# Optimization experiments

Hardware: AMD Instinct MI355X
Metric: run time of the kernel (lower is better)

Reference implementation:

```python
import jax, jax.numpy as jnp
import numpy as np

PATCH = 12
IN_CH = 1
EMBED = 96
K_NEIGH = 5
N_NODES = 1024
B = 4
L_TIME = 2016  # 12 * 168 patches
CIN = IN_CH * (K_NEIGH + 1)


def setup_inputs() -> dict:
    key = jax.random.key(0)
    k1, k2, k3, k4 = jax.random.split(key, 4)
    long_term_history = jax.random.normal(k1, (B, N_NODES, IN_CH, L_TIME), dtype=jnp.float32)
    # positive adjacency weights (used as multinomial sampling probabilities)
    adj_mx = jax.random.uniform(k2, (N_NODES, N_NODES), dtype=jnp.float32, minval=1e-3, maxval=1.0)
    # Conv2d(in=CIN, out=EMBED, kernel=(PATCH,1)) -> weight [EMBED, CIN, PATCH]
    conv_w = jax.random.normal(k3, (EMBED, CIN, PATCH), dtype=jnp.float32) * 0.02
    conv_b = jax.random.normal(k4, (EMBED,), dtype=jnp.float32) * 0.02
    return {"long_term_history": long_term_history, "adj_mx": adj_mx,
            "conv_w": conv_w, "conv_b": conv_b}


def _sample_k_neighbors(adj_mx, k, key):
    # per-row multinomial with replacement via the Gumbel-max trick
    logits = jnp.log(adj_mx)                      # row-normalization is a constant shift
    g = jax.random.gumbel(key, (adj_mx.shape[0], k, adj_mx.shape[1]), dtype=adj_mx.dtype)
    return jnp.argmax(logits[:, None, :] + g, axis=-1)  # [N, k] int


def reference(long_term_history, adj_mx, conv_w, conv_b):
    b, n, c, lt = long_term_history.shape
    # adj_adjust_u = 1, adj_adjust_v = 0 (adjust_adj_mx=False) -> adjusted adj == adj
    sampled = _sample_k_neighbors(adj_mx, K_NEIGH, jax.random.key(42))  # [N, K]
    # batched neighbor gather: [B, N, K, C, L] -> [B, N, K*C, L]
    nb = long_term_history[:, sampled].reshape(b, n, K_NEIGH * c, lt)
    data = jnp.concatenate([long_term_history, nb], axis=2)  # [B, N, (K+1)*C, L]
    # patchify conv: kernel (PATCH,1), stride (PATCH,1) == per-patch GEMM
    p = lt // PATCH
    patches = data.reshape(b, n, CIN, p, PATCH)              # [B,N,Cin,P,patch]
    out = jnp.einsum('bncpt,oct->bnop', patches, conv_w) + conv_b[None, None, :, None]
    return out  # [B, N, EMBED, P]
```

## Files before the change

kernel.cpp:

```cpp
#include <hip/hip_runtime.h>
#include <cstdint>
#include <cstddef>

#define N_NODES 1024
#define K_NEIGH 5
#define L_TIME  2016
#define PATCHSZ 12
#define EMBED   96
#define CINX    6
#define P_CNT   168
#define KDOT    72
#define OUT_PER_BN (EMBED * P_CNT)

#define WS_WH 24576
#define WS_WL (24576 + 18432)

typedef __attribute__((ext_vector_type(8))) short   bf16x8;
typedef __attribute__((ext_vector_type(4))) float   f32x4;
typedef __attribute__((ext_vector_type(4))) unsigned int u32x4;

__device__ __forceinline__ uint32_t f2bf_bits(float f) {
  uint32_t u = __float_as_uint(f);
  return (u + 0x7fffu + ((u >> 16) & 1u)) >> 16;
}
__device__ __forceinline__ float bf_hi_f(uint32_t hb) { return __uint_as_float(hb << 16); }

__device__ __forceinline__ uint32_t rotl32(uint32_t x, int r) {
  return (x << r) | (x >> (32 - r));
}
__device__ __forceinline__ uint32_t threefry_bits(uint32_t hi, uint32_t lo) {
  const uint32_t ks0 = 0u, ks1 = 42u;
  const uint32_t ks2 = ks0 ^ ks1 ^ 0x1BD11BDAu;
  uint32_t x0 = hi + ks0, x1 = lo + ks1;
#define TF_ROUND(r) { x0 += x1; x1 = rotl32(x1, (r)); x1 ^= x0; }
  TF_ROUND(13) TF_ROUND(15) TF_ROUND(26) TF_ROUND(6)
  x0 += ks1; x1 += ks2 + 1u;
  TF_ROUND(17) TF_ROUND(29) TF_ROUND(16) TF_ROUND(24)
  x0 += ks2; x1 += ks0 + 2u;
  TF_ROUND(13) TF_ROUND(15) TF_ROUND(26) TF_ROUND(6)
  x0 += ks0; x1 += ks1 + 3u;
  TF_ROUND(17) TF_ROUND(29) TF_ROUND(16) TF_ROUND(24)
  x0 += ks1; x1 += ks2 + 4u;
  TF_ROUND(13) TF_ROUND(15) TF_ROUND(26) TF_ROUND(6)
  x0 += ks2; x1 += ks0 + 5u;
#undef TF_ROUND
  return x0 ^ x1;
}
__device__ __forceinline__ float gumbel_from_bits(uint32_t bits) {
  float f = __uint_as_float((bits >> 9) | 0x3f800000u) - 1.0f;
  f = fmaxf(f, 1.17549435e-38f);
  return -logf(-logf(f));
}

__global__ __launch_bounds__(256)
void wpack_kernel(const float* __restrict__ wgt, char* __restrict__ ws) {
  const int tid = threadIdx.x;
  for (int t = tid; t < 1152; t += 256) {
    const int L  = t & 63;
    const int mk = t >> 6;
    const int kc = mk % 3;
    const int m  = mk / 3;
    const int o  = m * 16 + (L & 15);
    const int kbase = kc * 32 + (L >> 4) * 8;
    uint32_t hb[8], lb[8];
    #pragma unroll
    for (int j = 0; j < 8; ++j) {
      const int k = kbase + j;
      float v = (k < KDOT) ? wgt[o * KDOT + k] : 0.0f;
      hb[j] = f2bf_bits(v);
      lb[j] = f2bf_bits(v - bf_hi_f(hb[j]));
    }
    u32x4 ph, pl;
    #pragma unroll
    for (int i = 0; i < 4; ++i) {
      ph[i] = hb[2*i] | (hb[2*i+1] << 16);
      pl[i] = lb[2*i] | (lb[2*i+1] << 16);
    }
    *reinterpret_cast<u32x4*>(ws + WS_WH + mk * 1024 + L * 16) = ph;
    *reinterpret_cast<u32x4*>(ws + WS_WL + mk * 1024 + L * 16) = pl;
  }
}

__global__ __launch_bounds__(1024)
void sample_kernel(const float* __restrict__ adj, int* __restrict__ sampled) {
  const int n = blockIdx.x;
  const int tid = threadIdx.x;
  const float la = logf(adj[(size_t)n * N_NODES + tid]);

  float best[K_NEIGH];
  int   bestj[K_NEIGH];
  #pragma unroll
  for (int k = 0; k < K_NEIGH; ++k) {
    uint32_t bits = threefry_bits(0u, (uint32_t)((n * K_NEIGH + k) * N_NODES + tid));
    best[k] = la + gumbel_from_bits(bits);
    bestj[k] = tid;
  }
  #pragma unroll
  for (int k = 0; k < K_NEIGH; ++k) {
    #pragma unroll
    for (int off = 32; off > 0; off >>= 1) {
      float ov = __shfl_down(best[k], off);
      int   oj = __shfl_down(bestj[k], off);
      if (ov > best[k] || (ov == best[k] && oj < bestj[k])) { best[k] = ov; bestj[k] = oj; }
    }
  }
  __shared__ float sv[16][K_NEIGH];
  __shared__ int   sj[16][K_NEIGH];
  if ((tid & 63) == 0) {
    #pragma unroll
    for (int k = 0; k < K_NEIGH; ++k) { sv[tid >> 6][k] = best[k]; sj[tid >> 6][k] = bestj[k]; }
  }
  __syncthreads();
  if (tid < K_NEIGH) {
    float b = sv[0][tid];
    int  bj = sj[0][tid];
    #pragma unroll
    for (int w = 1; w < 16; ++w) {
      if (sv[w][tid] > b || (sv[w][tid] == b && sj[w][tid] < bj)) { b = sv[w][tid]; bj = sj[w][tid]; }
    }
    sampled[n * K_NEIGH + tid] = bj;
  }
}

__device__ __forceinline__ const float* sel_row(const float* r0, const float* r1,
                                                const float* r2, const float* r3,
                                                const float* r4, const float* r5,
                                                int c) {
  const float* p = r0;
  p = (c == 1) ? r1 : p;
  p = (c == 2) ? r2 : p;
  p = (c == 3) ? r3 : p;
  p = (c == 4) ? r4 : p;
  p = (c == 5) ? r5 : p;
  return p;
}

__global__ __launch_bounds__(256)
void embed_kernel(const float* __restrict__ hist, const char* __restrict__ ws,
                  const float* __restrict__ bias, const int* __restrict__ sampled,
                  float* __restrict__ out) {
  const int tid  = threadIdx.x;
  const int L    = tid & 63;
  const int wave = tid >> 6;
  const int g    = L >> 4;
  const int col  = L & 15;

  bf16x8 wh[18], wl[18];
  #pragma unroll
  for (int mk = 0; mk < 18; ++mk) {
    wh[mk] = __builtin_bit_cast(bf16x8, *reinterpret_cast<const u32x4*>(ws + WS_WH + mk*1024 + L*16));
    wl[mk] = __builtin_bit_cast(bf16x8, *reinterpret_cast<const u32x4*>(ws + WS_WL + mk*1024 + L*16));
  }
  f32x4 bv[6];
  #pragma unroll
  for (int m = 0; m < 6; ++m)
    #pragma unroll
    for (int i = 0; i < 4; ++i)
      bv[m][i] = bias[m * 16 + g * 4 + i];

  for (int bn = blockIdx.x; bn < 4 * N_NODES; bn += 512) {
    const int n = bn & (N_NODES - 1);
    const int b = bn >> 10;
    const float* r0 = hist + (size_t)bn * L_TIME;
    const float* r1 = hist + ((size_t)b * N_NODES + sampled[n * K_NEIGH + 0]) * L_TIME;
    const float* r2 = hist + ((size_t)b * N_NODES + sampled[n * K_NEIGH + 1]) * L_TIME;
    const float* r3 = hist + ((size_t)b * N_NODES + sampled[n * K_NEIGH + 2]) * L_TIME;
    const float* r4 = hist + ((size_t)b * N_NODES + sampled[n * K_NEIGH + 3]) * L_TIME;
    const float* r5 = hist + ((size_t)b * N_NODES + sampled[n * K_NEIGH + 4]) * L_TIME;
    float* outbn = out + (size_t)bn * OUT_PER_BN;

    const float* a0[3];
    const float* a1[3];
    bool okk[3];
    #pragma unroll
    for (int kc = 0; kc < 3; ++kc) {
      const int gk = kc * 32 + g * 8;
      okk[kc] = (gk < KDOT);
      const int c0 = gk / 12,       t0 = gk - c0 * 12;
      const int c1 = (gk + 4) / 12, t1 = (gk + 4) - c1 * 12;
      a0[kc] = sel_row(r0, r1, r2, r3, r4, r5, c0) + t0;
      a1[kc] = sel_row(r0, r1, r2, r3, r4, r5, c1) + t1;
    }

    for (int ntl = wave; ntl < 11; ntl += 4) {
      const int p = ntl * 16 + col;
      const bool pok = (p < P_CNT);
      f32x4 acc[6];
      #pragma unroll
      for (int m = 0; m < 6; ++m) acc[m] = bv[m];

      #pragma unroll
      for (int kc = 0; kc < 3; ++kc) {
        u32x4 ph = {0,0,0,0}, pl = {0,0,0,0};
        if (okk[kc] && pok) {
          const float4 f0 = *reinterpret_cast<const float4*>(a0[kc] + p * PATCHSZ);
          const float4 f1 = *reinterpret_cast<const float4*>(a1[kc] + p * PATCHSZ);
          const float v[8] = {f0.x, f0.y, f0.z, f0.w, f1.x, f1.y, f1.z, f1.w};
          uint32_t hb[8], lb[8];
          #pragma unroll
          for (int j = 0; j < 8; ++j) {
            hb[j] = f2bf_bits(v[j]);
            lb[j] = f2bf_bits(v[j] - bf_hi_f(hb[j]));
          }
          #pragma unroll
          for (int i = 0; i < 4; ++i) {
            ph[i] = hb[2*i] | (hb[2*i+1] << 16);
            pl[i] = lb[2*i] | (lb[2*i+1] << 16);
          }
        }
        const bf16x8 xh = __builtin_bit_cast(bf16x8, ph);
        const bf16x8 xl = __builtin_bit_cast(bf16x8, pl);
        #pragma unroll
        for (int m = 0; m < 6; ++m) {
          acc[m] = __builtin_amdgcn_mfma_f32_16x16x32_bf16(wh[m*3+kc], xh, acc[m], 0, 0, 0);
          acc[m] = __builtin_amdgcn_mfma_f32_16x16x32_bf16(wh[m*3+kc], xl, acc[m], 0, 0, 0);
          acc[m] = __builtin_amdgcn_mfma_f32_16x16x32_bf16(wl[m*3+kc], xh, acc[m], 0, 0, 0);
        }
      }
      if (pok) {
        #pragma unroll
        for (int m = 0; m < 6; ++m) {
          const int o = m * 16 + g * 4;
          #pragma unroll
          for (int i = 0; i < 4; ++i)
            __builtin_nontemporal_store(acc[m][i], &outbn[(size_t)(o + i) * P_CNT + p]);
        }
      }
    }
  }
}

extern "C" void kernel_launch(void* const* d_in, const int* in_sizes, int n_in,
                              void* d_out, int out_size, void* d_ws, size_t ws_size,
                              hipStream_t stream) {
  const float* hist = (const float*)d_in[0];
  const float* adj  = (const float*)d_in[1];
  const float* wgt  = (const float*)d_in[2];
  const float* bias = (const float*)d_in[3];
  float* out = (float*)d_out;
  char* ws   = (char*)d_ws;
  int* sampled = (int*)d_ws;

  wpack_kernel<<<dim3(1), dim3(256), 0, stream>>>(wgt, ws);
  sample_kernel<<<dim3(N_NODES), dim3(1024), 0, stream>>>(adj, sampled);
  embed_kernel<<<dim3(512), dim3(256), 0, stream>>>(hist, ws, bias, sampled, out);
}
```

Baseline: 461.7 us.

## Stage packed weights in LDS and launch one block per (batch,node)

Moves the packed hi/lo bf16 weight fragments and the bias from per-thread registers into shared memory. This frees registers so launch_bounds can request 4 blocks per SM, and each of the 4096 (batch,node) pairs now gets its own block instead of a grid-stride loop over 512 blocks. Row offsets become 32-bit indices, and the bias is added at store time instead of preloading the accumulators. In exchange, every block reloads 36KB of weights from global into LDS, and the inner MFMA loop now issues LDS reads.

Result: no change. 467.9 us (+1.3%).

```diff
diff --git a/kernel.cpp b/kernel.cpp
--- a/kernel.cpp
+++ b/kernel.cpp
@@ -122,11 +122,10 @@
   }
 }
 
-__device__ __forceinline__ const float* sel_row(const float* r0, const float* r1,
-                                                const float* r2, const float* r3,
-                                                const float* r4, const float* r5,
-                                                int c) {
-  const float* p = r0;
+__device__ __forceinline__ uint32_t sel6(uint32_t r0, uint32_t r1, uint32_t r2,
+                                         uint32_t r3, uint32_t r4, uint32_t r5,
+                                         int c) {
+  uint32_t p = r0;
   p = (c == 1) ? r1 : p;
   p = (c == 2) ? r2 : p;
   p = (c == 3) ? r3 : p;
@@ -135,66 +134,65 @@
   return p;
 }
 
-__global__ __launch_bounds__(256)
+__global__ __launch_bounds__(256, 4)
 void embed_kernel(const float* __restrict__ hist, const char* __restrict__ ws,
                   const float* __restrict__ bias, const int* __restrict__ sampled,
                   float* __restrict__ out) {
+  __shared__ __align__(16) char smem[36864 + 384];
+  u32x4* Wl = reinterpret_cast<u32x4*>(smem);
+  float* Bl = reinterpret_cast<float*>(smem + 36864);
+
   const int tid  = threadIdx.x;
   const int L    = tid & 63;
   const int wave = tid >> 6;
   const int g    = L >> 4;
   const int col  = L & 15;
 
-  bf16x8 wh[18], wl[18];
-  #pragma unroll
-  for (int mk = 0; mk < 18; ++mk) {
-    wh[mk] = __builtin_bit_cast(bf16x8, *reinterpret_cast<const u32x4*>(ws + WS_WH + mk*1024 + L*16));
-    wl[mk] = __builtin_bit_cast(bf16x8, *reinterpret_cast<const u32x4*>(ws + WS_WL + mk*1024 + L*16));
-  }
-  f32x4 bv[6];
-  #pragma unroll
-  for (int m = 0; m < 6; ++m)
-    #pragma unroll
-    for (int i = 0; i < 4; ++i)
-      bv[m][i] = bias[m * 16 + g * 4 + i];
-
-  for (int bn = blockIdx.x; bn < 4 * N_NODES; bn += 512) {
-    const int n = bn & (N_NODES - 1);
-    const int b = bn >> 10;
-    const float* r0 = hist + (size_t)bn * L_TIME;
-    const float* r1 = hist + ((size_t)b * N_NODES + sampled[n * K_NEIGH + 0]) * L_TIME;
-    const float* r2 = hist + ((size_t)b * N_NODES + sampled[n * K_NEIGH + 1]) * L_TIME;
-    const float* r3 = hist + ((size_t)b * N_NODES + sampled[n * K_NEIGH + 2]) * L_TIME;
-    const float* r4 = hist + ((size_t)b * N_NODES + sampled[n * K_NEIGH + 3]) * L_TIME;
-    const float* r5 = hist + ((size_t)b * N_NODES + sampled[n * K_NEIGH + 4]) * L_TIME;
-    float* outbn = out + (size_t)bn * OUT_PER_BN;
-
-    const float* a0[3];
-    const float* a1[3];
-    bool okk[3];
-    #pragma unroll
-    for (int kc = 0; kc < 3; ++kc) {
-      const int gk = kc * 32 + g * 8;
-      okk[kc] = (gk < KDOT);
-      const int c0 = gk / 12,       t0 = gk - c0 * 12;
-      const int c1 = (gk + 4) / 12, t1 = (gk + 4) - c1 * 12;
-      a0[kc] = sel_row(r0, r1, r2, r3, r4, r5, c0) + t0;
-      a1[kc] = sel_row(r0, r1, r2, r3, r4, r5, c1) + t1;
-    }
-
-    for (int ntl = wave; ntl < 11; ntl += 4) {
+  for (int i = tid; i < 2304; i += 256)
+    Wl[i] = *reinterpret_cast<const u32x4*>(ws + WS_WH + (size_t)i * 16);
+  if (tid < EMBED) Bl[tid] = bias[tid];
+
+  const int bn = blockIdx.x;
+  const int n  = bn & (N_NODES - 1);
+  const int b  = bn >> 10;
+
+  const uint32_t r0 = (uint32_t)bn * L_TIME;
+  const uint32_t r1 = ((uint32_t)b * N_NODES + (uint32_t)sampled[n * K_NEIGH + 0]) * L_TIME;
+  const uint32_t r2 = ((uint32_t)b * N_NODES + (uint32_t)sampled[n * K_NEIGH + 1]) * L_TIME;
+  const uint32_t r3 = ((uint32_t)b * N_NODES + (uint32_t)sampled[n * K_NEIGH + 2]) * L_TIME;
+  const uint32_t r4 = ((uint32_t)b * N_NODES + (uint32_t)sampled[n * K_NEIGH + 3]) * L_TIME;
+  const uint32_t r5 = ((uint32_t)b * N_NODES + (uint32_t)sampled[n * K_NEIGH + 4]) * L_TIME;
+
+  uint32_t o0[3], o1[3];
+  #pragma unroll
+  for (int kc = 0; kc < 3; ++kc) {
+    const int gk = kc * 32 + g * 8;
+    const int c0 = gk / 12,       t0 = gk - c0 * 12;
+    const int c1 = (gk + 4) / 12, t1 = (gk + 4) - c1 * 12;
+    o0[kc] = sel6(r0, r1, r2, r3, r4, r5, c0) + (uint32_t)t0;
+    o1[kc] = sel6(r0, r1, r2, r3, r4, r5, c1) + (uint32_t)t1;
+  }
+
+  __syncthreads();
+
+  float* outbn = out + (size_t)bn * OUT_PER_BN;
+
+  #pragma unroll
+  for (int t = 0; t < 3; ++t) {
+    const int ntl = wave * 3 + t;
+    if (ntl < 11) {
       const int p = ntl * 16 + col;
       const bool pok = (p < P_CNT);
       f32x4 acc[6];
       #pragma unroll
-      for (int m = 0; m < 6; ++m) acc[m] = bv[m];
+      for (int m = 0; m < 6; ++m) acc[m] = {0.f, 0.f, 0.f, 0.f};
 
       #pragma unroll
       for (int kc = 0; kc < 3; ++kc) {
         u32x4 ph = {0,0,0,0}, pl = {0,0,0,0};
-        if (okk[kc] && pok) {
-          const float4 f0 = *reinterpret_cast<const float4*>(a0[kc] + p * PATCHSZ);
-          const float4 f1 = *reinterpret_cast<const float4*>(a1[kc] + p * PATCHSZ);
+        if (pok && (kc < 2 || g == 0)) {
+          const float4 f0 = *reinterpret_cast<const float4*>(hist + o0[kc] + (uint32_t)p * PATCHSZ);
+          const float4 f1 = *reinterpret_cast<const float4*>(hist + o1[kc] + (uint32_t)p * PATCHSZ);
           const float v[8] = {f0.x, f0.y, f0.z, f0.w, f1.x, f1.y, f1.z, f1.w};
           uint32_t hb[8], lb[8];
           #pragma unroll
@@ -212,18 +210,22 @@
         const bf16x8 xl = __builtin_bit_cast(bf16x8, pl);
         #pragma unroll
         for (int m = 0; m < 6; ++m) {
-          acc[m] = __builtin_amdgcn_mfma_f32_16x16x32_bf16(wh[m*3+kc], xh, acc[m], 0, 0, 0);
-          acc[m] = __builtin_amdgcn_mfma_f32_16x16x32_bf16(wh[m*3+kc], xl, acc[m], 0, 0, 0);
-          acc[m] = __builtin_amdgcn_mfma_f32_16x16x32_bf16(wl[m*3+kc], xh, acc[m], 0, 0, 0);
+          const int mk = m * 3 + kc;
+          const bf16x8 whf = __builtin_bit_cast(bf16x8, Wl[mk * 64 + L]);
+          const bf16x8 wlf = __builtin_bit_cast(bf16x8, Wl[1152 + mk * 64 + L]);
+          acc[m] = __builtin_amdgcn_mfma_f32_16x16x32_bf16(whf, xh, acc[m], 0, 0, 0);
+          acc[m] = __builtin_amdgcn_mfma_f32_16x16x32_bf16(whf, xl, acc[m], 0, 0, 0);
+          acc[m] = __builtin_amdgcn_mfma_f32_16x16x32_bf16(wlf, xh, acc[m], 0, 0, 0);
         }
       }
       if (pok) {
         #pragma unroll
         for (int m = 0; m < 6; ++m) {
-          const int o = m * 16 + g * 4;
+          const f32x4 bb = *reinterpret_cast<const f32x4*>(&Bl[m * 16 + g * 4]);
           #pragma unroll
           for (int i = 0; i < 4; ++i)
-            __builtin_nontemporal_store(acc[m][i], &outbn[(size_t)(o + i) * P_CNT + p]);
+            __builtin_nontemporal_store(acc[m][i] + bb[i],
+                                        &outbn[(size_t)(m * 16 + g * 4 + i) * P_CNT + p]);
         }
       }
     }
@@ -243,5 +245,5 @@
 
   wpack_kernel<<<dim3(1), dim3(256), 0, stream>>>(wgt, ws);
   sample_kernel<<<dim3(N_NODES), dim3(1024), 0, stream>>>(adj, sampled);
-  embed_kernel<<<dim3(512), dim3(256), 0, stream>>>(hist, ws, bias, sampled, out);
-}
+  embed_kernel<<<dim3(4 * N_NODES), dim3(256), 0, stream>>>(hist, ws, bias, sampled, out);
+}
```
